# Optimization experiments

Hardware: AMD Instinct MI355X
Metric: run time of the kernel (lower is better)

## Reference

```python
import jax, jax.numpy as jnp
import numpy as np

B, N, C = 8, 2048, 320
CQ = C // 5  # query/key channel dim = 64


def setup_inputs() -> dict:
    key = jax.random.key(0)
    ks = jax.random.split(key, 8)
    s = 0.05
    return {
        "x": jax.random.normal(ks[0], (B, N, C), dtype=jnp.float32),
        "Wq": jax.random.normal(ks[1], (CQ, C), dtype=jnp.float32) * s,
        "bq": jax.random.normal(ks[2], (CQ,), dtype=jnp.float32) * s,
        "Wk": jax.random.normal(ks[3], (CQ, C), dtype=jnp.float32) * s,
        "bk": jax.random.normal(ks[4], (CQ,), dtype=jnp.float32) * s,
        "Wv": jax.random.normal(ks[5], (C, C), dtype=jnp.float32) * s,
        "bv": jax.random.normal(ks[6], (C,), dtype=jnp.float32) * s,
        "gamma": jnp.zeros((1,), dtype=jnp.float32) + 0.5,
    }


def reference(x, Wq, bq, Wk, bk, Wv, bv, gamma):
    # x: (B, N, C). torch module permutes to (B, C, N) and uses 1x1 Conv1d,
    # which is a per-position linear over channels.
    q = jnp.einsum("bnc,qc->bnq", x, Wq) + bq          # (B, N, CQ) proj_query
    k = jnp.einsum("bnc,qc->bqn", x, Wk) + bk[:, None]  # (B, CQ, N) proj_key
    energy = jnp.einsum("bnq,bqm->bnm", q, k)           # (B, N, N)
    attention = jax.nn.softmax(energy, axis=-1)          # softmax over last dim
    v = jnp.einsum("bnc,dc->bdn", x, Wv) + bv[:, None]  # (B, C, N) proj_value
    # torch: out = bmm(V (B,C,N), A (B,N,N)) -> out[b,c,n] = sum_k V[b,c,k]*A[b,k,n]
    out = jnp.einsum("bck,bkn->bcn", v, attention)       # (B, C, N)
    out = gamma[0] * out + jnp.swapaxes(x, 1, 2)         # residual on (B, C, N)
    return jnp.swapaxes(out, 1, 2)                       # (B, N, C)
```

## Files before the change

### kernel.cpp

```cpp
#include <hip/hip_runtime.h>
#include <hip/hip_bf16.h>

#define BB 8
#define NN 2048
#define CC 320
#define CQ 64
#define LOG2E 1.4426950408889634f

typedef __attribute__((ext_vector_type(8)))  short bf16x8;
typedef __attribute__((ext_vector_type(4)))  float f32x4;
typedef __attribute__((ext_vector_type(16))) float f32x16;
typedef __attribute__((ext_vector_type(4)))  unsigned short us4;
typedef __attribute__((ext_vector_type(8)))  unsigned short us8;
typedef __attribute__((ext_vector_type(4)))  unsigned int u32x4;
typedef unsigned short u16;


static __device__ __forceinline__ u16 f2b(float f) {
  unsigned u = __builtin_bit_cast(unsigned, f);
  unsigned r = (u + 0x7FFFu + ((u >> 16) & 1u)) >> 16;
  return (u16)r;
}
static __device__ __forceinline__ float b2f(u16 s) {
  unsigned u = ((unsigned)s) << 16;
  return __builtin_bit_cast(float, u);
}

static __device__ __forceinline__ f32x16 zero16() {
  f32x16 v = {0,0,0,0, 0,0,0,0, 0,0,0,0, 0,0,0,0};
  return v;
}
static __device__ __forceinline__ f32x4 zero4() {
  f32x4 v = {0,0,0,0};
  return v;
}

static __device__ __forceinline__ void gll16(const void* g, void* l) {
  __builtin_amdgcn_global_load_lds(
      (const __attribute__((address_space(1))) unsigned int*)g,
      (__attribute__((address_space(3))) unsigned int*)l, 16, 0, 0);
}

static __device__ __forceinline__ bf16x8 cvt8(float4 a, float4 b) {
  unsigned p0, p1, p2, p3;
  asm("v_cvt_pk_bf16_f32 %0, %1, %2" : "=v"(p0) : "v"(a.x), "v"(a.y));
  asm("v_cvt_pk_bf16_f32 %0, %1, %2" : "=v"(p1) : "v"(a.z), "v"(a.w));
  asm("v_cvt_pk_bf16_f32 %0, %1, %2" : "=v"(p2) : "v"(b.x), "v"(b.y));
  asm("v_cvt_pk_bf16_f32 %0, %1, %2" : "=v"(p3) : "v"(b.z), "v"(b.w));
  u32x4 w = {p0, p1, p2, p3};
  return __builtin_bit_cast(bf16x8, w);
}

__global__ __launch_bounds__(256) void cvt_x_blk(const float* __restrict__ x,
                                                 u16* __restrict__ X3) {
  __shared__ float xs[32][324];
  const int t = threadIdx.x;
  const int b = blockIdx.x;
  const size_t srcb = (size_t)b * 32 * CC;
#pragma unroll
  for (int i = 0; i < 10; ++i) {
    const int lidx = i * 256 + t;
    const int m = lidx / 80;
    const int kq = lidx - m * 80;
    float4 v = *(const float4*)(x + srcb + (size_t)m * CC + kq * 4);
    *(float4*)&xs[m][kq * 4] = v;
  }
  __syncthreads();
  u16* dst0 = X3 + (size_t)b * 10240;
#pragma unroll
  for (int i = 0; i < 5; ++i) {
    const int u = i * 256 + t;
    const int kk8 = u >> 5, ml = u & 31;
    float4 a = *(const float4*)&xs[ml][kk8 * 8];
    float4 c = *(const float4*)&xs[ml][kk8 * 8 + 4];
    bf16x8 o = cvt8(a, c);
    *(bf16x8*)(dst0 + (size_t)u * 8) = o;
  }
}

__global__ __launch_bounds__(256) void cvt_w_blk(const float* __restrict__ Wq,
                                                 const float* __restrict__ Wk,
                                                 const float* __restrict__ Wv,
                                                 u16* __restrict__ W3) {
  __shared__ float xs[32][324];
  const int t = threadIdx.x;
  const int b = blockIdx.x;
#pragma unroll
  for (int i = 0; i < 10; ++i) {
    const int lidx = i * 256 + t;
    const int m = lidx / 80;
    const int kq = lidx - m * 80;
    const int row = b * 32 + m;
    const float* src = (row < 64) ? (Wq + (size_t)row * CC)
                     : (row < 128) ? (Wk + (size_t)(row - 64) * CC)
                                   : (Wv + (size_t)(row - 128) * CC);
    float4 v = *(const float4*)(src + kq * 4);
    *(float4*)&xs[m][kq * 4] = v;
  }
  __syncthreads();
  u16* dst0 = W3 + (size_t)b * 10240;
#pragma unroll
  for (int i = 0; i < 5; ++i) {
    const int u = i * 256 + t;
    const int kk8 = u >> 5, ml = u & 31;
    float4 a = *(const float4*)&xs[ml][kk8 * 8];
    float4 c = *(const float4*)&xs[ml][kk8 * 8 + 4];
    bf16x8 o = cvt8(a, c);
    *(bf16x8*)(dst0 + (size_t)u * 8) = o;
  }
}

__global__ __launch_bounds__(256) void gemm_qkv(
    const u16* __restrict__ X3, const u16* __restrict__ W3,
    const float* __restrict__ bq, const float* __restrict__ bk,
    const float* __restrict__ bv,
    u16* __restrict__ Qb, u16* __restrict__ Kb, u16* __restrict__ Vt) {
  const int tid = threadIdx.x;
  const int lane = tid & 63, wid = tid >> 6;
  const int r = lane & 31, h = lane >> 5;
  const int bid = blockIdx.x;
  const int xcd = bid & 7;
  const int slot = bid >> 3;
  const int colt = slot % 7;
  const int yG = slot / 7;
  const int ytile = yG * 8 + xcd;
  const int m0 = ytile * 128 + wid * 32;
  const int col0 = colt * 64;
  const int mt = m0 >> 5;

  const u16* abase  = X3 + (size_t)mt * 10240 + (size_t)h * 256 + r * 8;
  const u16* b0base = W3 + (size_t)(colt * 2) * 10240 + (size_t)h * 256 + r * 8;
  const u16* b1base = b0base + 10240;

  f32x16 acc0 = zero16(), acc1 = zero16();
  bf16x8 a   = *(const bf16x8*)(abase);
  bf16x8 b0v = *(const bf16x8*)(b0base);
  bf16x8 b1v = *(const bf16x8*)(b1base);
#pragma unroll 1
  for (int ks = 0; ks < 20; ++ks) {
    bf16x8 na, nb0, nb1;
    if (ks < 19) {
      na  = *(const bf16x8*)(abase  + (ks + 1) * 512);
      nb0 = *(const bf16x8*)(b0base + (ks + 1) * 512);
      nb1 = *(const bf16x8*)(b1base + (ks + 1) * 512);
    }
    acc0 = __builtin_amdgcn_mfma_f32_32x32x16_bf16(a, b0v, acc0, 0, 0, 0);
    acc1 = __builtin_amdgcn_mfma_f32_32x32x16_bf16(a, b1v, acc1, 0, 0, 0);
    a = na; b0v = nb0; b1v = nb1;
  }

  const int bb = m0 >> 11;
  const int mloc = m0 & 2047;

#pragma unroll
  for (int nt = 0; nt < 2; ++nt) {
    const int col = col0 + nt * 32 + r;
    const f32x16 A = nt ? acc1 : acc0;
    if (col0 >= 128) {
      const int c = col - 128;
      const float bias = bv[c];
      u16* vdst = Vt + (((size_t)(bb * 256 + (mloc >> 3)) * 320 + c) * 8) + 4 * h;
#pragma unroll
      for (int g = 0; g < 4; ++g) {
        us4 o;
#pragma unroll
        for (int e = 0; e < 4; ++e) o[e] = f2b(A[g * 4 + e] + bias);
        *(us4*)(vdst + (size_t)g * 2560) = o;
      }
    } else if (col0 >= 64) {
      const float bias = bk[col - 64];
#pragma unroll
      for (int reg = 0; reg < 16; ++reg) {
        const int row = m0 + (reg & 3) + 8 * (reg >> 2) + 4 * h;
        Kb[(size_t)row * CQ + (col - 64)] = f2b(A[reg] + bias);
      }
    } else {
      const float bias = bq[col];
      const int kt = mloc >> 5;
      u16* qdst = Qb + (((size_t)(bb * 64 + kt) * 8 + (col >> 3)) * 32) * 8 + (col & 7);
#pragma unroll
      for (int reg = 0; reg < 16; ++reg) {
        const int kl = (reg & 3) + 8 * (reg >> 2) + 4 * h;
        qdst[kl * 8] = f2b((A[reg] + bias) * LOG2E);
      }
    }
  }
}

__global__ __launch_bounds__(512) void row_stats(
    const u16* __restrict__ Qb, const u16* __restrict__ Kb,
    u16* __restrict__ Vt) {
  __shared__ float Sp[8][64];
  __shared__ float sInv[64];
  const int tid = threadIdx.x;
  const int lane = tid & 63, wid = tid >> 6;
  const int rl = lane & 15, hq = lane >> 4;
  const int bid = blockIdx.x;
  const int batch = bid & 7;
  const int kloc64 = (bid >> 3) * 64;

  bf16x8 af[4][2];
#pragma unroll
  for (int mt = 0; mt < 4; ++mt) {
    const int k_loc = kloc64 + mt * 16 + rl;
    const int kt = k_loc >> 5, kl = k_loc & 31;
#pragma unroll
    for (int qs = 0; qs < 2; ++qs)
      af[mt][qs] = *(const bf16x8*)(Qb +
          (((size_t)(batch * 64 + kt) * 8 + qs * 4 + hq) * 32 + kl) * 8);
  }

  float S[4][4];
#pragma unroll
  for (int mt = 0; mt < 4; ++mt)
#pragma unroll
    for (int rr = 0; rr < 4; ++rr) S[mt][rr] = 0.f;

  const int mstart = batch * NN + wid * 256;
  const u16* kr = Kb + (size_t)(mstart + rl) * CQ + hq * 8;
  bf16x8 c0 = *(const bf16x8*)(kr);
  bf16x8 c1 = *(const bf16x8*)(kr + 32);
#pragma unroll 1
  for (int ms = 0; ms < 16; ++ms) {
    bf16x8 n0, n1;
    if (ms < 15) {
      n0 = *(const bf16x8*)(kr + 16 * CQ);
      n1 = *(const bf16x8*)(kr + 16 * CQ + 32);
    }
#pragma unroll
    for (int mt = 0; mt < 4; ++mt) {
      f32x4 e = zero4();
      e = __builtin_amdgcn_mfma_f32_16x16x32_bf16(af[mt][0], c0, e, 0, 0, 0);
      e = __builtin_amdgcn_mfma_f32_16x16x32_bf16(af[mt][1], c1, e, 0, 0, 0);
#pragma unroll
      for (int rr = 0; rr < 4; ++rr) S[mt][rr] += __builtin_amdgcn_exp2f(e[rr]);
    }
    c0 = n0; c1 = n1; kr += 16 * CQ;
  }

#pragma unroll
  for (int d = 1; d < 16; d <<= 1)
#pragma unroll
    for (int mt = 0; mt < 4; ++mt)
#pragma unroll
      for (int rr = 0; rr < 4; ++rr) S[mt][rr] += __shfl_xor(S[mt][rr], d, 64);

  if (rl == 0) {
#pragma unroll
    for (int mt = 0; mt < 4; ++mt)
#pragma unroll
      for (int rr = 0; rr < 4; ++rr) Sp[wid][mt * 16 + hq * 4 + rr] = S[mt][rr];
  }
  __syncthreads();
  if (tid < 64) {
    float s = 0.f;
#pragma unroll
    for (int p = 0; p < 8; ++p) s += Sp[p][tid];
    sInv[tid] = 1.0f / s;
  }
  __syncthreads();

  const int kt8b = kloc64 >> 3;
#pragma unroll 1
  for (int i = 0; i < 10; ++i) {
    const int chunk = i * 512 + tid;
    const int kt8l = chunk / 640;
    const int rem = chunk - kt8l * 640;
    const int c = rem >> 1;
    const int h2 = rem & 1;
    u16* p = Vt + (((size_t)(batch * 256 + kt8b + kt8l) * 320 + c) * 8) + h2 * 4;
    us4 v = *(const us4*)p;
    us4 o;
#pragma unroll
    for (int e2 = 0; e2 < 4; ++e2) o[e2] = f2b(b2f(v[e2]) * sInv[kt8l * 8 + h2 * 4 + e2]);
    *(us4*)p = o;
  }
}

__global__ __launch_bounds__(256, 2) void attn(
    const u16* __restrict__ Qb, const u16* __restrict__ Kb,
    const u16* __restrict__ Vt, const float* __restrict__ x,
    const float* __restrict__ gamma, float* __restrict__ out) {
  __shared__ __align__(16) char LDSRAW[57344];
  const int tid = threadIdx.x;
  const int lane = tid & 63, wid = tid >> 6;
  const int wn = wid >> 1;
  const int kh = wid & 1;
  const int r = lane & 31, h = lane >> 5;
  const int bid = blockIdx.x;
  const int b = bid & 7;
  const int rest = bid >> 3;
  const int ch = rest & 1;
  const int n0 = (rest >> 1) * 64;

  bf16x8 kf[4];
  {
    const u16* krow = Kb + (size_t)(b * NN + n0 + wn * 32 + r) * CQ + h * 8;
#pragma unroll
    for (int qs = 0; qs < 4; ++qs) kf[qs] = *(const bf16x8*)(krow + qs * 16);
  }

  f32x16 acc[5];
#pragma unroll
  for (int j = 0; j < 5; ++j) acc[j] = zero16();

#define STAGE(TN, BUF) {                                                       \
    _Pragma("unroll")                                                          \
    for (int i_ = 0; i_ < 7; ++i_) {                                           \
      const int c_ = wid * 7 + i_;                                             \
      const int khc_ = c_ / 14;                                                \
      const int rem_ = c_ % 14;                                                \
      char* dst_ = LDSRAW + (BUF) * 28672 + khc_ * 14336 + rem_ * 1024;        \
      if (rem_ < 4) {                                                          \
        const u16* src_ = Qb + ((size_t)(b * 64 + khc_ * 32 + (TN)) * 2048)    \
                             + rem_ * 512 + lane * 8;                          \
        gll16(src_, dst_);                                                     \
      } else {                                                                 \
        const int v_ = rem_ - 4;                                               \
        const int off_ = v_ * 512 + lane * 8;                                  \
        const int row_ = off_ / 1280;                                          \
        const int win_ = off_ - row_ * 1280;                                   \
        const u16* src_ = Vt +                                                 \
            ((size_t)(b * 256 + khc_ * 128 + (TN) * 4 + row_) * 320            \
             + ch * 160) * 8 + win_;                                           \
        gll16(src_, dst_);                                                     \
      }                                                                        \
    }                                                                          \
  }

#define COMPUTE(T) {                                                           \
    const char* base_ = LDSRAW + ((T) & 1) * 28672 + kh * 14336;               \
    bf16x8 qf[4];                                                              \
    _Pragma("unroll")                                                          \
    for (int qs = 0; qs < 4; ++qs)                                             \
      qf[qs] = *(const bf16x8*)(base_ + (qs * 2 + h) * 512 + r * 16);          \
    f32x16 e = zero16();                                                       \
    _Pragma("unroll")                                                          \
    for (int qs = 0; qs < 4; ++qs)                                             \
      e = __builtin_amdgcn_mfma_f32_32x32x16_bf16(qf[qs], kf[qs], e, 0, 0, 0); \
    bf16x8 vf[5][2];                                                           \
    _Pragma("unroll")                                                          \
    for (int j = 0; j < 5; ++j)                                                \
      _Pragma("unroll")                                                        \
      for (int ks = 0; ks < 2; ++ks)                                           \
        vf[j][ks] = *(const bf16x8*)(base_ + 4096 + (ks * 2 + h) * 2560        \
                                     + (j * 32 + r) * 16);                     \
    unsigned pk0, pk1, pk2, pk3, pk4, pk5, pk6, pk7;                           \
    { float l0 = __builtin_amdgcn_exp2f(e[0]),  h0 = __builtin_amdgcn_exp2f(e[1]);  \
      float l1 = __builtin_amdgcn_exp2f(e[2]),  h1 = __builtin_amdgcn_exp2f(e[3]);  \
      float l2 = __builtin_amdgcn_exp2f(e[4]),  h2 = __builtin_amdgcn_exp2f(e[5]);  \
      float l3 = __builtin_amdgcn_exp2f(e[6]),  h3 = __builtin_amdgcn_exp2f(e[7]);  \
      float l4 = __builtin_amdgcn_exp2f(e[8]),  h4 = __builtin_amdgcn_exp2f(e[9]);  \
      float l5 = __builtin_amdgcn_exp2f(e[10]), h5 = __builtin_amdgcn_exp2f(e[11]); \
      float l6 = __builtin_amdgcn_exp2f(e[12]), h6 = __builtin_amdgcn_exp2f(e[13]); \
      float l7 = __builtin_amdgcn_exp2f(e[14]), h7 = __builtin_amdgcn_exp2f(e[15]); \
      asm("v_cvt_pk_bf16_f32 %0, %1, %2" : "=v"(pk0) : "v"(l0), "v"(h0));      \
      asm("v_cvt_pk_bf16_f32 %0, %1, %2" : "=v"(pk1) : "v"(l1), "v"(h1));      \
      asm("v_cvt_pk_bf16_f32 %0, %1, %2" : "=v"(pk2) : "v"(l2), "v"(h2));      \
      asm("v_cvt_pk_bf16_f32 %0, %1, %2" : "=v"(pk3) : "v"(l3), "v"(h3));      \
      asm("v_cvt_pk_bf16_f32 %0, %1, %2" : "=v"(pk4) : "v"(l4), "v"(h4));      \
      asm("v_cvt_pk_bf16_f32 %0, %1, %2" : "=v"(pk5) : "v"(l5), "v"(h5));      \
      asm("v_cvt_pk_bf16_f32 %0, %1, %2" : "=v"(pk6) : "v"(l6), "v"(h6));      \
      asm("v_cvt_pk_bf16_f32 %0, %1, %2" : "=v"(pk7) : "v"(l7), "v"(h7)); }    \
    asm("v_permlane32_swap_b32 %0, %1" : "+v"(pk0), "+v"(pk2));                \
    asm("v_permlane32_swap_b32 %0, %1" : "+v"(pk1), "+v"(pk3));                \
    asm("v_permlane32_swap_b32 %0, %1" : "+v"(pk4), "+v"(pk6));                \
    asm("v_permlane32_swap_b32 %0, %1" : "+v"(pk5), "+v"(pk7));                \
    u32x4 w0_ = {pk0, pk1, pk2, pk3};                                          \
    u32x4 w1_ = {pk4, pk5, pk6, pk7};                                          \
    bf16x8 pa0 = __builtin_bit_cast(bf16x8, w0_);                              \
    bf16x8 pa1 = __builtin_bit_cast(bf16x8, w1_);                              \
    _Pragma("unroll")                                                          \
    for (int j = 0; j < 5; ++j) {                                              \
      acc[j] = __builtin_amdgcn_mfma_f32_32x32x16_bf16(pa0, vf[j][0], acc[j], 0, 0, 0); \
      acc[j] = __builtin_amdgcn_mfma_f32_32x32x16_bf16(pa1, vf[j][1], acc[j], 0, 0, 0); \
    }                                                                          \
  }

  STAGE(0, 0);
  __syncthreads();
#pragma unroll 1
  for (int t = 0; t < 32; ++t) {
    if (t < 31) STAGE(t + 1, (t + 1) & 1);
    COMPUTE(t);
    __syncthreads();
  }
#undef STAGE
#undef COMPUTE

  float* red = (float*)LDSRAW;
  if (kh == 1) {
#pragma unroll
    for (int reg = 0; reg < 16; ++reg) {
      const int nl = (reg & 3) + 8 * (reg >> 2) + 4 * h;
#pragma unroll
      for (int j = 0; j < 5; ++j)
        red[wn * 5120 + nl * 160 + j * 32 + r] = acc[j][reg];
    }
  }
  __syncthreads();
  if (kh == 0) {
    const float g = gamma[0];
#pragma unroll
    for (int reg = 0; reg < 16; ++reg) {
      const int nl = (reg & 3) + 8 * (reg >> 2) + 4 * h;
      const size_t rowb = ((size_t)(b * NN) + n0 + wn * 32 + nl) * CC + ch * 160 + r;
#pragma unroll
      for (int j = 0; j < 5; ++j) {
        const size_t idx = rowb + (size_t)(j * 32);
        const float s = acc[j][reg] + red[wn * 5120 + nl * 160 + j * 32 + r];
        out[idx] = g * s + x[idx];
      }
    }
  }
}

extern "C" void kernel_launch(void* const* d_in, const int* in_sizes, int n_in,
                              void* d_out, int out_size, void* d_ws, size_t ws_size,
                              hipStream_t stream) {
  const float* x     = (const float*)d_in[0];
  const float* Wq    = (const float*)d_in[1];
  const float* bq    = (const float*)d_in[2];
  const float* Wk    = (const float*)d_in[3];
  const float* bk    = (const float*)d_in[4];
  const float* Wv    = (const float*)d_in[5];
  const float* bv    = (const float*)d_in[6];
  const float* gamma = (const float*)d_in[7];
  float* out = (float*)d_out;

  char* w = (char*)d_ws;
  u16* X3 = (u16*)(w);
  u16* W3 = (u16*)(w + 10485760);
  u16* Qb = (u16*)(w + 10772480);
  u16* Kb = (u16*)(w + 12869632);
  u16* Vt = (u16*)(w + 14966784);

  cvt_x_blk<<<512, 256, 0, stream>>>(x, X3);
  cvt_w_blk<<<14, 256, 0, stream>>>(Wq, Wk, Wv, W3);
  gemm_qkv<<<896, 256, 0, stream>>>(X3, W3, bq, bk, bv, Qb, Kb, Vt);
  row_stats<<<256, 512, 0, stream>>>(Qb, Kb, Vt);
  attn<<<512, 256, 0, stream>>>(Qb, Kb, Vt, x, gamma, out);
}
```

Before: 90.67 us.

## Load Q fragments directly to registers, stage only V through LDS

Q tiles are no longer staged through shared memory. Each wave now loads its Q fragments straight from global memory into registers, one tile ahead, and ping-pongs between two register sets inside a manually unrolled-by-two loop. This shrinks the LDS footprint from 56KB to 40KB and cuts LDS traffic and staging instructions per iteration. The cost is higher register pressure and global-load latency that must now be hidden by the register prefetch. It also relies on a Q layout in global memory that matches the fragment addressing.

```diff
diff --git a/kernel.cpp b/kernel.cpp
--- a/kernel.cpp
+++ b/kernel.cpp
@@ -281,7 +281,7 @@
     const u16* __restrict__ Qb, const u16* __restrict__ Kb,
     const u16* __restrict__ Vt, const float* __restrict__ x,
     const float* __restrict__ gamma, float* __restrict__ out) {
-  __shared__ __align__(16) char LDSRAW[57344];
+  __shared__ __align__(16) char LDSRAW[40960];
   const int tid = threadIdx.x;
   const int lane = tid & 63, wid = tid >> 6;
   const int wn = wid >> 1;
@@ -304,46 +304,44 @@
 #pragma unroll
   for (int j = 0; j < 5; ++j) acc[j] = zero16();
 
+  const u16* qb3 = Qb + ((size_t)(b * 64 + kh * 32) * 8) * 256 + (size_t)r * 8;
+
 #define STAGE(TN, BUF) {                                                       \
     _Pragma("unroll")                                                          \
-    for (int i_ = 0; i_ < 7; ++i_) {                                           \
-      const int c_ = wid * 7 + i_;                                             \
-      const int khc_ = c_ / 14;                                                \
-      const int rem_ = c_ % 14;                                                \
-      char* dst_ = LDSRAW + (BUF) * 28672 + khc_ * 14336 + rem_ * 1024;        \
-      if (rem_ < 4) {                                                          \
-        const u16* src_ = Qb + ((size_t)(b * 64 + khc_ * 32 + (TN)) * 2048)    \
-                             + rem_ * 512 + lane * 8;                          \
-        gll16(src_, dst_);                                                     \
-      } else {                                                                 \
-        const int v_ = rem_ - 4;                                               \
-        const int off_ = v_ * 512 + lane * 8;                                  \
-        const int row_ = off_ / 1280;                                          \
-        const int win_ = off_ - row_ * 1280;                                   \
-        const u16* src_ = Vt +                                                 \
-            ((size_t)(b * 256 + khc_ * 128 + (TN) * 4 + row_) * 320            \
-             + ch * 160) * 8 + win_;                                           \
-        gll16(src_, dst_);                                                     \
-      }                                                                        \
+    for (int i_ = 0; i_ < 5; ++i_) {                                           \
+      const int c_ = wid * 5 + i_;                                             \
+      const int khc_ = c_ / 10;                                                \
+      const int rem_ = c_ % 10;                                                \
+      char* dst_ = LDSRAW + (BUF) * 20480 + khc_ * 10240 + rem_ * 1024;        \
+      const int off_ = rem_ * 512 + lane * 8;                                  \
+      const int row_ = off_ / 1280;                                            \
+      const int win_ = off_ - row_ * 1280;                                     \
+      const u16* src_ = Vt +                                                   \
+          ((size_t)(b * 256 + khc_ * 128 + (TN) * 4 + row_) * 320              \
+           + ch * 160) * 8 + win_;                                             \
+      gll16(src_, dst_);                                                       \
     }                                                                          \
   }
 
-#define COMPUTE(T) {                                                           \
-    const char* base_ = LDSRAW + ((T) & 1) * 28672 + kh * 14336;               \
-    bf16x8 qf[4];                                                              \
+#define LQ(QN, TN) {                                                           \
     _Pragma("unroll")                                                          \
     for (int qs = 0; qs < 4; ++qs)                                             \
-      qf[qs] = *(const bf16x8*)(base_ + (qs * 2 + h) * 512 + r * 16);          \
+      QN[qs] = *(const bf16x8*)(qb3 + ((size_t)(TN) * 8 + qs * 2 + h) * 256);  \
+  }
+
+#define COMPUTE(T, BUF, QF, QN, TNX) {                                         \
+    LQ(QN, TNX)                                                                \
+    const char* base_ = LDSRAW + (BUF) * 20480 + kh * 10240;                   \
     f32x16 e = zero16();                                                       \
     _Pragma("unroll")                                                          \
     for (int qs = 0; qs < 4; ++qs)                                             \
-      e = __builtin_amdgcn_mfma_f32_32x32x16_bf16(qf[qs], kf[qs], e, 0, 0, 0); \
+      e = __builtin_amdgcn_mfma_f32_32x32x16_bf16(QF[qs], kf[qs], e, 0, 0, 0); \
     bf16x8 vf[5][2];                                                           \
     _Pragma("unroll")                                                          \
     for (int j = 0; j < 5; ++j)                                                \
       _Pragma("unroll")                                                        \
       for (int ks = 0; ks < 2; ++ks)                                           \
-        vf[j][ks] = *(const bf16x8*)(base_ + 4096 + (ks * 2 + h) * 2560        \
+        vf[j][ks] = *(const bf16x8*)(base_ + (ks * 2 + h) * 2560               \
                                      + (j * 32 + r) * 16);                     \
     unsigned pk0, pk1, pk2, pk3, pk4, pk5, pk6, pk7;                           \
     { float l0 = __builtin_amdgcn_exp2f(e[0]),  h0 = __builtin_amdgcn_exp2f(e[1]);  \
@@ -377,15 +375,22 @@
     }                                                                          \
   }
 
+  bf16x8 qfA[4], qfB[4];
+
   STAGE(0, 0);
+  LQ(qfA, 0)
   __syncthreads();
 #pragma unroll 1
-  for (int t = 0; t < 32; ++t) {
-    if (t < 31) STAGE(t + 1, (t + 1) & 1);
-    COMPUTE(t);
+  for (int t = 0; t < 32; t += 2) {
+    STAGE(t + 1, 1);
+    COMPUTE(t, 0, qfA, qfB, t + 1);
     __syncthreads();
+    if (t + 2 < 32) STAGE(t + 2, 0);
+    COMPUTE(t + 1, 1, qfB, qfA, (t + 2) & 31);
+    __syncthreads();
   }
 #undef STAGE
+#undef LQ
 #undef COMPUTE
 
   float* red = (float*)LDSRAW;
```

Result: faster. 87.11 us (-3.9%).
